# Kernel optimization log

Hardware: AMD Instinct MI355X
Metric: run time of the kernel (lower is better)

Reference implementation:

```python
import jax, jax.numpy as jnp
import numpy as np

ATOM = 34
HID = 256
LATENT = 128
CELLS = 512
B, N = 64, 128
NEG = -9e15


def setup_inputs() -> dict:
    key = jax.random.key(0)
    ks = jax.random.split(key, 20)
    inp = {}
    inp["xs"] = jax.random.normal(ks[0], (B, N, ATOM), dtype=jnp.float32)
    inp["A"] = jax.random.randint(ks[1], (B, N, N), 0, 2, dtype=jnp.int32)
    inp["cell_emb"] = jax.random.normal(ks[2], (B, CELLS), dtype=jnp.float32)
    inp["Wg"] = jax.random.normal(ks[3], (3, ATOM, ATOM), dtype=jnp.float32) * 0.17
    inp["bg"] = jnp.zeros((3, ATOM), dtype=jnp.float32)
    inp["attn"] = jax.random.normal(ks[4], (3, 2 * ATOM), dtype=jnp.float32) * 0.17
    # W_gnn_trans: 34 -> 256
    inp["Wt"] = jax.random.normal(ks[5], (ATOM, HID), dtype=jnp.float32) * 0.08
    inp["bt"] = jnp.zeros((HID,), dtype=jnp.float32)
    # ffn: 256 -> 34 ; ffn2: 34 -> latent
    inp["Wf"] = jax.random.normal(ks[6], (HID, ATOM), dtype=jnp.float32) * 0.08
    inp["bf"] = jnp.zeros((ATOM,), dtype=jnp.float32)
    inp["Wf2"] = jax.random.normal(ks[7], (ATOM, LATENT), dtype=jnp.float32) * 0.11
    inp["bf2"] = jnp.zeros((LATENT,), dtype=jnp.float32)
    # Decoder MLP: (latent+cells)->128->256->512->1
    din = LATENT + CELLS
    inp["W1"] = jax.random.normal(ks[8], (din, 128), dtype=jnp.float32) * 0.05
    inp["b1"] = jnp.zeros((128,), dtype=jnp.float32)
    inp["W2"] = jax.random.normal(ks[9], (128, 256), dtype=jnp.float32) * 0.07
    inp["b2"] = jnp.zeros((256,), dtype=jnp.float32)
    inp["W3"] = jax.random.normal(ks[10], (256, 512), dtype=jnp.float32) * 0.05
    inp["b3"] = jnp.zeros((512,), dtype=jnp.float32)
    inp["W4"] = jax.random.normal(ks[11], (512, 1), dtype=jnp.float32) * 0.06
    inp["b4"] = jnp.zeros((1,), dtype=jnp.float32)
    return inp


def reference(xs, A, cell_emb, Wg, bg, attn, Wt, bt, Wf, bf, Wf2, bf2,
              W1, b1, W2, b2, W3, b3, W4, b4):
    # ---- gnn(): 3 rounds of GAT-style masked-softmax message passing ----
    # a_input[b,p,q] = [h[b,p], h[b,q]], so e = leaky_relu(h@a1 outer+ h@a2)
    h0 = xs
    mask = A > 0  # [B,N,N]
    x = xs
    for i in range(3):
        h = jax.nn.relu(jnp.einsum('bnd,de->bne', x, Wg[i]) + bg[i])  # [B,N,34]
        f_src = h @ attn[i, :ATOM]   # [B,N] -- score contribution of row atom
        f_dst = h @ attn[i, ATOM:]   # [B,N] -- score contribution of col atom
        e = jax.nn.leaky_relu(f_src[:, :, None] + f_dst[:, None, :], 0.01)
        scores = jnp.where(mask, e, NEG)
        att = jax.nn.softmax(scores, axis=2)  # dropout disabled (deterministic)
        x = x + jnp.einsum('bpq,bqd->bpd', att, h)
    g = jax.nn.relu(jnp.einsum('bnd,dh->bnh', x, Wt) + bt)  # [B,N,HID]

    # ---- VEC_forward ----
    d = jnp.einsum('bnh,hd->bnd', g, Wf) + bf + h0        # ffn + residual to input xs
    d = jnp.einsum('bnd,dl->bnl', d, Wf2) + bf2           # [B,N,LATENT]
    d = jnp.max(d, axis=1)                                # [B,LATENT]
    vec = jax.nn.sigmoid(jnp.concatenate([d, cell_emb], axis=-1))

    # ---- Decoder_mlp (dropout disabled) ----
    hminus = jax.nn.relu(vec @ W1 + b1)
    hminus = jax.nn.relu(hminus @ W2 + b2)
    hminus = jax.nn.relu(hminus @ W3 + b3)
    score = hminus @ W4 + b4                              # [B,1]
    return score
```

## Files before the change

kernel.cpp:

```cpp
#include <hip/hip_runtime.h>

constexpr int ATOM = 34;
constexpr int HID = 256;
constexpr int LATENT = 128;
constexpr int CELLS = 512;
constexpr int NN = 128;
constexpr int NA = NN * ATOM;
#define NEGF (-9e15f)

__global__ __launch_bounds__(256, 2) void k_gat(
    const float* __restrict__ xsrc, const int* __restrict__ A,
    const float* __restrict__ Wg, const float* __restrict__ bg,
    const float* __restrict__ av, float* __restrict__ X)
{
    const int b = blockIdx.x >> 3, s8 = blockIdx.x & 7;
    const int t = threadIdx.x, lane = t & 63, wave = t >> 6;
    const int p0 = s8 * 16;

    __shared__ __align__(16) float xl[NN * 36];
    __shared__ __align__(16) float hlT[ATOM * 132];
    __shared__ __align__(16) float att[16 * NN];
    __shared__ __align__(16) float wgT[ATOM * 36];
    __shared__ float fs[NN], fd[NN], bgs[ATOM], avs[2 * ATOM];

    for (int i = t; i < ATOM * ATOM; i += 256) {
        int d = i / ATOM, e = i - d * ATOM;
        wgT[e * 36 + d] = Wg[i];
    }
    if (t < 68)  wgT[(t >> 1) * 36 + 34 + (t & 1)] = 0.f;
    if (t < ATOM)     bgs[t] = bg[t];
    if (t < 2 * ATOM) avs[t] = av[t];
    const float* xp = xsrc + b * NA;
    for (int i = t; i < NA; i += 256) xl[(i / ATOM) * 36 + (i % ATOM)] = xp[i];
    xl[(t >> 1) * 36 + 34 + (t & 1)] = 0.f;
    __syncthreads();

    {
        const int n = t >> 1, sub = t & 1;
        float xr[36];
        {
            float4* xr4 = (float4*)xr;
            const float4* p4 = (const float4*)(xl + n * 36);
            #pragma unroll
            for (int k = 0; k < 9; ++k) xr4[k] = p4[k];
        }
        #pragma unroll
        for (int j = 0; j < 17; ++j) {
            const int e = sub + 2 * j;
            float acc = bgs[e];
            const float4* wp = (const float4*)(wgT + e * 36);
            #pragma unroll
            for (int k = 0; k < 9; ++k) {
                float4 w = wp[k];
                acc += xr[4*k] * w.x + xr[4*k+1] * w.y + xr[4*k+2] * w.z + xr[4*k+3] * w.w;
            }
            hlT[e * 132 + n] = fmaxf(acc, 0.f);
        }
    }
    __syncthreads();

    {
        const int n = t & 127, w = t >> 7;
        const float* avp = avs + w * ATOM;
        float acc = 0.f;
        #pragma unroll
        for (int d = 0; d < ATOM; ++d) acc += hlT[d * 132 + n] * avp[d];
        if (w == 0) fs[n] = acc; else fd[n] = acc;
    }
    __syncthreads();

    const int* Ab = A + b * NN * NN;
    #pragma unroll
    for (int i = 0; i < 4; ++i) {
        int lp = wave * 4 + i, gp = p0 + lp;
        float fsv = fs[gp];
        unsigned long long m0 = __ballot(Ab[gp * NN + lane] > 0);
        unsigned long long m1 = __ballot(Ab[gp * NN + 64 + lane] > 0);
        float s0 = fsv + fd[lane];
        s0 = (s0 > 0.f) ? s0 : 0.01f * s0;
        if (!((m0 >> lane) & 1ull)) s0 = NEGF;
        float s1 = fsv + fd[64 + lane];
        s1 = (s1 > 0.f) ? s1 : 0.01f * s1;
        if (!((m1 >> lane) & 1ull)) s1 = NEGF;
        float mx = fmaxf(s0, s1);
        #pragma unroll
        for (int o = 32; o >= 1; o >>= 1) mx = fmaxf(mx, __shfl_xor(mx, o, 64));
        float e0 = __expf(s0 - mx), e1 = __expf(s1 - mx);
        float sm = e0 + e1;
        #pragma unroll
        for (int o = 32; o >= 1; o >>= 1) sm += __shfl_xor(sm, o, 64);
        float inv = 1.f / sm;
        att[lp * NN + lane]      = e0 * inv;
        att[lp * NN + 64 + lane] = e1 * inv;
    }
    __syncthreads();

    {
        const int p = t >> 4, g = t & 15, gp = p0 + p;
        const float4* ap  = (const float4*)(att + p * NN);
        const float4* h1p = (const float4*)(hlT + g * 132);
        const float4* h2p = (const float4*)(hlT + (g + 16) * 132);
        float a1 = 0.f, a2 = 0.f;
        #pragma unroll 8
        for (int k = 0; k < 32; ++k) {
            float4 a4 = ap[k], x1 = h1p[k], x2 = h2p[k];
            a1 += a4.x * x1.x + a4.y * x1.y + a4.z * x1.z + a4.w * x1.w;
            a2 += a4.x * x2.x + a4.y * x2.y + a4.z * x2.z + a4.w * x2.w;
        }
        float* Xr = X + b * NA + gp * ATOM;
        Xr[g]      = xl[gp * 36 + g] + a1;
        Xr[g + 16] = xl[gp * 36 + g + 16] + a2;
        if (g < 2) {
            const float4* h3p = (const float4*)(hlT + (g + 32) * 132);
            float a3 = 0.f;
            #pragma unroll 8
            for (int k = 0; k < 32; ++k) {
                float4 a4 = ap[k], x3 = h3p[k];
                a3 += a4.x * x3.x + a4.y * x3.y + a4.z * x3.z + a4.w * x3.w;
            }
            Xr[g + 32] = xl[gp * 36 + g + 32] + a3;
        }
    }
}

__global__ __launch_bounds__(512, 2) void k_phaseB(
    const float* __restrict__ X, const float* __restrict__ xs,
    const float* __restrict__ Wt, const float* __restrict__ bt,
    const float* __restrict__ Wf, const float* __restrict__ bf,
    const float* __restrict__ Wf2, const float* __restrict__ bf2,
    float* __restrict__ DM)
{
    const int b = blockIdx.x >> 2, q4 = blockIdx.x & 3;
    const int t = threadIdx.x;
    const int p0 = q4 * 32;
    __shared__ float wt[HID * 36];
    __shared__ float wf[HID * 36];
    __shared__ float xl[32][36];
    __shared__ float dlT[ATOM][33];
    __shared__ float wf2s[ATOM * LATENT];
    __shared__ float bts[HID];
    __shared__ float bfs[ATOM];
    __shared__ float sl[512];

    for (int i = t; i < ATOM * HID; i += 512) {
        int d = i >> 8, h = i & 255;
        wt[h * 36 + d] = Wt[i];
    }
    for (int i = t; i < HID * ATOM; i += 512) {
        int h = i / ATOM, j = i % ATOM;
        wf[h * 36 + j] = Wf[i];
    }
    for (int i = t; i < ATOM * LATENT; i += 512) wf2s[i] = Wf2[i];
    if (t < HID)  bts[t] = bt[t];
    if (t < ATOM) bfs[t] = bf[t];
    for (int i = t; i < 32 * ATOM; i += 512) xl[i / ATOM][i % ATOM] = X[b * NA + p0 * ATOM + i];
    __syncthreads();

    const int row = t & 31, sub = t >> 5;
    float dp[ATOM];
    #pragma unroll
    for (int j = 0; j < ATOM; ++j) dp[j] = 0.f;
    {
        float xr[36];
        float4* xr4 = (float4*)xr;
        const float4* xlr = (const float4*)&xl[row][0];
        #pragma unroll
        for (int k = 0; k < 9; ++k) xr4[k] = xlr[k];
        for (int i = 0; i < 16; ++i) {
            const int h = sub + 16 * i;
            float acc = bts[h];
            const float4* wtp = (const float4*)&wt[h * 36];
            #pragma unroll
            for (int k = 0; k < 8; ++k) {
                float4 w4 = wtp[k];
                acc += xr[4*k] * w4.x + xr[4*k+1] * w4.y + xr[4*k+2] * w4.z + xr[4*k+3] * w4.w;
            }
            acc += xr[32] * wt[h * 36 + 32] + xr[33] * wt[h * 36 + 33];
            acc = fmaxf(acc, 0.f);
            const float4* wfp = (const float4*)&wf[h * 36];
            #pragma unroll
            for (int k = 0; k < 8; ++k) {
                float4 w4 = wfp[k];
                dp[4*k]   += acc * w4.x; dp[4*k+1] += acc * w4.y;
                dp[4*k+2] += acc * w4.z; dp[4*k+3] += acc * w4.w;
            }
            dp[32] += acc * wf[h * 36 + 32];
            dp[33] += acc * wf[h * 36 + 33];
        }
    }
    __syncthreads();
    {
        float* pl = (sub < 8) ? wt : wf;
        const int s8 = sub & 7;
        #pragma unroll
        for (int j = 0; j < ATOM; ++j) pl[(s8 * 32 + row) * ATOM + j] = dp[j];
    }
    __syncthreads();
    for (int i = t; i < 32 * ATOM; i += 512) {
        int rr = i / ATOM, j = i % ATOM;
        float dv = bfs[j] + xs[b * NA + (p0 + rr) * ATOM + j];
        #pragma unroll
        for (int s = 0; s < 8; ++s)
            dv += wt[(s * 32 + rr) * ATOM + j] + wf[(s * 32 + rr) * ATOM + j];
        dlT[j][rr] = dv;
    }
    __syncthreads();
    {
        const int l = t & 127, chunk = t >> 7;
        float w2r[ATOM];
        #pragma unroll
        for (int j = 0; j < ATOM; ++j) w2r[j] = wf2s[j * LATENT + l];
        float mx = -3.4e38f;
        for (int rr = chunk * 8; rr < chunk * 8 + 8; ++rr) {
            float acc = bf2[l];
            #pragma unroll
            for (int j = 0; j < ATOM; ++j) acc += dlT[j][rr] * w2r[j];
            mx = fmaxf(mx, acc);
        }
        sl[chunk * 128 + l] = mx;
    }
    __syncthreads();
    if (t < LATENT)
        DM[(b * 4 + q4) * LATENT + t] =
            fmaxf(fmaxf(sl[t], sl[128 + t]), fmaxf(sl[256 + t], sl[384 + t]));
}

__global__ __launch_bounds__(1024) void k_dec(
    const float* __restrict__ DM, const float* __restrict__ cell,
    const float* __restrict__ W1, const float* __restrict__ b1,
    const float* __restrict__ W2, const float* __restrict__ b2,
    const float* __restrict__ W3, const float* __restrict__ b3,
    const float* __restrict__ W4, const float* __restrict__ b4,
    float* __restrict__ out)
{
    const int b = blockIdx.x, t = threadIdx.x, lane = t & 63, wave = t >> 6;
    __shared__ float vec[LATENT + CELLS];
    __shared__ float h1[128], h2[256], h3[512];
    __shared__ float sl[1024];
    if (t < LATENT) {
        float m = fmaxf(fmaxf(DM[(b*4+0)*LATENT + t], DM[(b*4+1)*LATENT + t]),
                        fmaxf(DM[(b*4+2)*LATENT + t], DM[(b*4+3)*LATENT + t]));
        vec[t] = 1.f / (1.f + __expf(-m));
    } else if (t >= 512) {
        int c = t - 512;
        vec[LATENT + c] = 1.f / (1.f + __expf(-cell[b * CELLS + c]));
    }
    __syncthreads();
    {
        const int j = t & 127, part = t >> 7;
        float acc = 0.f;
        #pragma unroll 4
        for (int k = part * 80; k < part * 80 + 80; ++k)
            acc += vec[k] * W1[k * 128 + j];
        sl[part * 128 + j] = acc;
    }
    __syncthreads();
    if (t < 128) {
        float v = b1[t];
        #pragma unroll
        for (int p = 0; p < 8; ++p) v += sl[p * 128 + t];
        h1[t] = fmaxf(v, 0.f);
    }
    __syncthreads();
    {
        const int j = t & 255, part = t >> 8;
        float acc = 0.f;
        #pragma unroll 4
        for (int k = part * 32; k < part * 32 + 32; ++k)
            acc += h1[k] * W2[k * 256 + j];
        sl[part * 256 + j] = acc;
    }
    __syncthreads();
    if (t < 256) h2[t] = fmaxf(sl[t] + sl[256 + t] + sl[512 + t] + sl[768 + t] + b2[t], 0.f);
    __syncthreads();
    {
        const int j = t & 511, part = t >> 9;
        float acc = 0.f;
        #pragma unroll 4
        for (int k = part * 128; k < part * 128 + 128; ++k)
            acc += h2[k] * W3[k * 512 + j];
        sl[part * 512 + j] = acc;
    }
    __syncthreads();
    if (t < 512) h3[t] = fmaxf(sl[t] + sl[512 + t] + b3[t], 0.f);
    __syncthreads();
    float v = (t < 512) ? h3[t] * W4[t] : 0.f;
    #pragma unroll
    for (int o = 32; o >= 1; o >>= 1) v += __shfl_xor(v, o, 64);
    if (lane == 0) sl[wave] = v;
    __syncthreads();
    if (t == 0) {
        float s = b4[0];
        #pragma unroll
        for (int w = 0; w < 16; ++w) s += sl[w];
        out[b] = s;
    }
}

extern "C" void kernel_launch(void* const* d_in, const int* in_sizes, int n_in,
                              void* d_out, int out_size, void* d_ws, size_t ws_size,
                              hipStream_t stream) {
    const float* xs       = (const float*)d_in[0];
    const int*   A        = (const int*)  d_in[1];
    const float* cell_emb = (const float*)d_in[2];
    const float* Wg       = (const float*)d_in[3];
    const float* bg       = (const float*)d_in[4];
    const float* attnv    = (const float*)d_in[5];
    const float* Wt       = (const float*)d_in[6];
    const float* bt       = (const float*)d_in[7];
    const float* Wf       = (const float*)d_in[8];
    const float* bf       = (const float*)d_in[9];
    const float* Wf2      = (const float*)d_in[10];
    const float* bf2      = (const float*)d_in[11];
    const float* W1       = (const float*)d_in[12];
    const float* b1       = (const float*)d_in[13];
    const float* W2       = (const float*)d_in[14];
    const float* b2       = (const float*)d_in[15];
    const float* W3       = (const float*)d_in[16];
    const float* b3       = (const float*)d_in[17];
    const float* W4       = (const float*)d_in[18];
    const float* b4       = (const float*)d_in[19];
    float* out = (float*)d_out;

    float* W  = (float*)d_ws;
    float* X0 = W;
    float* X1 = W + 278528;
    float* DM = W + 557056;

    k_gat<<<512, 256, 0, stream>>>(xs, A, Wg,                   bg,            attnv,           X0);
    k_gat<<<512, 256, 0, stream>>>(X0, A, Wg + ATOM * ATOM,     bg + ATOM,     attnv + 2*ATOM,  X1);
    k_gat<<<512, 256, 0, stream>>>(X1, A, Wg + 2 * ATOM * ATOM, bg + 2 * ATOM, attnv + 4*ATOM,  X0);
    k_phaseB<<<256, 512, 0, stream>>>(X0, xs, Wt, bt, Wf, bf, Wf2, bf2, DM);
    k_dec<<<64, 1024, 0, stream>>>(DM, cell_emb, W1, b1, W2, b2, W3, b3, W4, b4, out);
}
```

Measured before the change: 177.8 us.

## Pack adjacency into bitmasks once and retile GAT blocks to 32 rows

The first GAT round writes the adjacency row masks as 64-bit ballots to workspace, and the later two rounds read those masks instead of reloading the int32 adjacency matrix. GAT blocks grow to 512 threads covering 32 rows each, which halves the number of blocks that recompute h for the same batch. The aggregation now uses a 2x2 register tile with a split-K shuffle reduction. phaseB drops its Wf2 and bias shared-memory staging in favour of direct global reads and zero-pads the weight rows. The cost is fewer blocks (256) and larger per-block work, which may reduce occupancy and latency hiding.

```diff
diff --git a/kernel.cpp b/kernel.cpp
--- a/kernel.cpp
+++ b/kernel.cpp
@@ -8,60 +8,62 @@
 constexpr int NA = NN * ATOM;
 #define NEGF (-9e15f)
 
-__global__ __launch_bounds__(256, 2) void k_gat(
+template <int R>
+__global__ __launch_bounds__(512) void k_gat(
     const float* __restrict__ xsrc, const int* __restrict__ A,
-    const float* __restrict__ Wg, const float* __restrict__ bg,
-    const float* __restrict__ av, float* __restrict__ X)
+    unsigned long long* __restrict__ Mm,
+    const float* __restrict__ Wgr, const float* __restrict__ bgr,
+    const float* __restrict__ avr, float* __restrict__ X)
 {
-    const int b = blockIdx.x >> 3, s8 = blockIdx.x & 7;
+    const int b = blockIdx.x >> 2, q4 = blockIdx.x & 3;
     const int t = threadIdx.x, lane = t & 63, wave = t >> 6;
-    const int p0 = s8 * 16;
+    const int p0 = q4 * 32;
 
     __shared__ __align__(16) float xl[NN * 36];
     __shared__ __align__(16) float hlT[ATOM * 132];
-    __shared__ __align__(16) float att[16 * NN];
+    __shared__ __align__(16) float att[32 * 132];
     __shared__ __align__(16) float wgT[ATOM * 36];
-    __shared__ float fs[NN], fd[NN], bgs[ATOM], avs[2 * ATOM];
-
-    for (int i = t; i < ATOM * ATOM; i += 256) {
+    __shared__ float fs[NN], fd[NN];
+
+    const float* xp = xsrc + b * NA;
+    for (int i = t; i < NA; i += 512) xl[(i / ATOM) * 36 + (i % ATOM)] = xp[i];
+    if (t < 256) xl[(t >> 1) * 36 + 34 + (t & 1)] = 0.f;
+    for (int i = t; i < ATOM * ATOM; i += 512) {
         int d = i / ATOM, e = i - d * ATOM;
-        wgT[e * 36 + d] = Wg[i];
-    }
-    if (t < 68)  wgT[(t >> 1) * 36 + 34 + (t & 1)] = 0.f;
-    if (t < ATOM)     bgs[t] = bg[t];
-    if (t < 2 * ATOM) avs[t] = av[t];
-    const float* xp = xsrc + b * NA;
-    for (int i = t; i < NA; i += 256) xl[(i / ATOM) * 36 + (i % ATOM)] = xp[i];
-    xl[(t >> 1) * 36 + 34 + (t & 1)] = 0.f;
-    __syncthreads();
-
-    {
-        const int n = t >> 1, sub = t & 1;
+        wgT[e * 36 + d] = Wgr[i];
+    }
+    if (t < 68) wgT[(t >> 1) * 36 + 34 + (t & 1)] = 0.f;
+    __syncthreads();
+
+    {
+        const int n = t >> 2, sub = t & 3;
         float xr[36];
         {
-            float4* xr4 = (float4*)xr;
+            float4* x4 = (float4*)xr;
             const float4* p4 = (const float4*)(xl + n * 36);
             #pragma unroll
-            for (int k = 0; k < 9; ++k) xr4[k] = p4[k];
-        }
-        #pragma unroll
-        for (int j = 0; j < 17; ++j) {
-            const int e = sub + 2 * j;
-            float acc = bgs[e];
-            const float4* wp = (const float4*)(wgT + e * 36);
-            #pragma unroll
-            for (int k = 0; k < 9; ++k) {
-                float4 w = wp[k];
-                acc += xr[4*k] * w.x + xr[4*k+1] * w.y + xr[4*k+2] * w.z + xr[4*k+3] * w.w;
+            for (int k = 0; k < 9; ++k) x4[k] = p4[k];
+        }
+        #pragma unroll
+        for (int j = 0; j < 9; ++j) {
+            const int e = sub + 4 * j;
+            if (e < ATOM) {
+                float acc = bgr[e];
+                const float4* wp = (const float4*)(wgT + e * 36);
+                #pragma unroll
+                for (int k = 0; k < 9; ++k) {
+                    float4 w = wp[k];
+                    acc += xr[4*k] * w.x + xr[4*k+1] * w.y + xr[4*k+2] * w.z + xr[4*k+3] * w.w;
+                }
+                hlT[e * 132 + n] = fmaxf(acc, 0.f);
             }
-            hlT[e * 132 + n] = fmaxf(acc, 0.f);
-        }
-    }
-    __syncthreads();
-
-    {
+        }
+    }
+    __syncthreads();
+
+    if (t < 2 * NN) {
         const int n = t & 127, w = t >> 7;
-        const float* avp = avs + w * ATOM;
+        const float* avp = avr + w * ATOM;
         float acc = 0.f;
         #pragma unroll
         for (int d = 0; d < ATOM; ++d) acc += hlT[d * 132 + n] * avp[d];
@@ -70,12 +72,20 @@
     __syncthreads();
 
     const int* Ab = A + b * NN * NN;
+    unsigned long long* Mb = Mm + b * NN * 2;
     #pragma unroll
     for (int i = 0; i < 4; ++i) {
-        int lp = wave * 4 + i, gp = p0 + lp;
-        float fsv = fs[gp];
-        unsigned long long m0 = __ballot(Ab[gp * NN + lane] > 0);
-        unsigned long long m1 = __ballot(Ab[gp * NN + 64 + lane] > 0);
+        const int lp = wave * 4 + i, gp = p0 + lp;
+        unsigned long long m0, m1;
+        if (R == 0) {
+            m0 = __ballot(Ab[gp * NN + lane] > 0);
+            m1 = __ballot(Ab[gp * NN + 64 + lane] > 0);
+            if (lane == 0) { Mb[gp * 2] = m0; Mb[gp * 2 + 1] = m1; }
+        } else {
+            m0 = Mb[gp * 2];
+            m1 = Mb[gp * 2 + 1];
+        }
+        const float fsv = fs[gp];
         float s0 = fsv + fd[lane];
         s0 = (s0 > 0.f) ? s0 : 0.01f * s0;
         if (!((m0 >> lane) & 1ull)) s0 = NEGF;
@@ -90,40 +100,60 @@
         #pragma unroll
         for (int o = 32; o >= 1; o >>= 1) sm += __shfl_xor(sm, o, 64);
         float inv = 1.f / sm;
-        att[lp * NN + lane]      = e0 * inv;
-        att[lp * NN + 64 + lane] = e1 * inv;
-    }
-    __syncthreads();
-
-    {
-        const int p = t >> 4, g = t & 15, gp = p0 + p;
-        const float4* ap  = (const float4*)(att + p * NN);
-        const float4* h1p = (const float4*)(hlT + g * 132);
-        const float4* h2p = (const float4*)(hlT + (g + 16) * 132);
-        float a1 = 0.f, a2 = 0.f;
-        #pragma unroll 8
-        for (int k = 0; k < 32; ++k) {
-            float4 a4 = ap[k], x1 = h1p[k], x2 = h2p[k];
-            a1 += a4.x * x1.x + a4.y * x1.y + a4.z * x1.z + a4.w * x1.w;
-            a2 += a4.x * x2.x + a4.y * x2.y + a4.z * x2.z + a4.w * x2.w;
-        }
-        float* Xr = X + b * NA + gp * ATOM;
-        Xr[g]      = xl[gp * 36 + g] + a1;
-        Xr[g + 16] = xl[gp * 36 + g + 16] + a2;
-        if (g < 2) {
-            const float4* h3p = (const float4*)(hlT + (g + 32) * 132);
-            float a3 = 0.f;
-            #pragma unroll 8
-            for (int k = 0; k < 32; ++k) {
-                float4 a4 = ap[k], x3 = h3p[k];
-                a3 += a4.x * x3.x + a4.y * x3.y + a4.z * x3.z + a4.w * x3.w;
-            }
-            Xr[g + 32] = xl[gp * 36 + g + 32] + a3;
+        att[lp * 132 + lane]      = e0 * inv;
+        att[lp * 132 + 64 + lane] = e1 * inv;
+    }
+    __syncthreads();
+
+    {
+        const int pq = t >> 5, g = (t >> 1) & 15, kh = t & 1;
+        const int rA = 2 * pq, rB = rA + 1;
+        const float4* apA = (const float4*)(att + rA * 132 + kh * 64);
+        const float4* apB = (const float4*)(att + rB * 132 + kh * 64);
+        const float4* hA  = (const float4*)(hlT + g * 132 + kh * 64);
+        const float4* hB  = (const float4*)(hlT + (g + 16) * 132 + kh * 64);
+        float aAA = 0.f, aAB = 0.f, aBA = 0.f, aBB = 0.f;
+        #pragma unroll
+        for (int k = 0; k < 16; ++k) {
+            float4 a0 = apA[k], a1 = apB[k], h0 = hA[k], h1 = hB[k];
+            aAA += a0.x * h0.x + a0.y * h0.y + a0.z * h0.z + a0.w * h0.w;
+            aAB += a0.x * h1.x + a0.y * h1.y + a0.z * h1.z + a0.w * h1.w;
+            aBA += a1.x * h0.x + a1.y * h0.y + a1.z * h0.z + a1.w * h0.w;
+            aBB += a1.x * h1.x + a1.y * h1.y + a1.z * h1.z + a1.w * h1.w;
+        }
+        aAA += __shfl_xor(aAA, 1, 64);
+        aAB += __shfl_xor(aAB, 1, 64);
+        aBA += __shfl_xor(aBA, 1, 64);
+        aBB += __shfl_xor(aBB, 1, 64);
+        if (kh == 0) {
+            const int gpA = p0 + rA, gpB = p0 + rB;
+            float* XrA = X + b * NA + gpA * ATOM;
+            float* XrB = X + b * NA + gpB * ATOM;
+            XrA[g]      = xl[gpA * 36 + g] + aAA;
+            XrA[g + 16] = xl[gpA * 36 + g + 16] + aAB;
+            XrB[g]      = xl[gpB * 36 + g] + aBA;
+            XrB[g + 16] = xl[gpB * 36 + g + 16] + aBB;
+        }
+    }
+    if (t < 128) {
+        const int p = t >> 2, c = 32 + ((t >> 1) & 1), kh = t & 1;
+        const float4* ap = (const float4*)(att + p * 132 + kh * 64);
+        const float4* hp = (const float4*)(hlT + c * 132 + kh * 64);
+        float a = 0.f;
+        #pragma unroll
+        for (int k = 0; k < 16; ++k) {
+            float4 a4 = ap[k], h4 = hp[k];
+            a += a4.x * h4.x + a4.y * h4.y + a4.z * h4.z + a4.w * h4.w;
+        }
+        a += __shfl_xor(a, 1, 64);
+        if (kh == 0) {
+            const int gp = p0 + p;
+            X[b * NA + gp * ATOM + c] = xl[gp * 36 + c] + a;
         }
     }
 }
 
-__global__ __launch_bounds__(512, 2) void k_phaseB(
+__global__ __launch_bounds__(512, 1) void k_phaseB(
     const float* __restrict__ X, const float* __restrict__ xs,
     const float* __restrict__ Wt, const float* __restrict__ bt,
     const float* __restrict__ Wf, const float* __restrict__ bf,
@@ -133,13 +163,10 @@
     const int b = blockIdx.x >> 2, q4 = blockIdx.x & 3;
     const int t = threadIdx.x;
     const int p0 = q4 * 32;
-    __shared__ float wt[HID * 36];
-    __shared__ float wf[HID * 36];
-    __shared__ float xl[32][36];
-    __shared__ float dlT[ATOM][33];
-    __shared__ float wf2s[ATOM * LATENT];
-    __shared__ float bts[HID];
-    __shared__ float bfs[ATOM];
+    __shared__ __align__(16) float wt[HID * 36];
+    __shared__ __align__(16) float wf[HID * 36];
+    __shared__ __align__(16) float xl[32 * 36];
+    __shared__ float dlT[ATOM * 33];
     __shared__ float sl[512];
 
     for (int i = t; i < ATOM * HID; i += 512) {
@@ -147,74 +174,81 @@
         wt[h * 36 + d] = Wt[i];
     }
     for (int i = t; i < HID * ATOM; i += 512) {
-        int h = i / ATOM, j = i % ATOM;
+        int h = i / ATOM, j = i - (i / ATOM) * ATOM;
         wf[h * 36 + j] = Wf[i];
     }
-    for (int i = t; i < ATOM * LATENT; i += 512) wf2s[i] = Wf2[i];
-    if (t < HID)  bts[t] = bt[t];
-    if (t < ATOM) bfs[t] = bf[t];
-    for (int i = t; i < 32 * ATOM; i += 512) xl[i / ATOM][i % ATOM] = X[b * NA + p0 * ATOM + i];
-    __syncthreads();
-
-    const int row = t & 31, sub = t >> 5;
-    float dp[ATOM];
-    #pragma unroll
-    for (int j = 0; j < ATOM; ++j) dp[j] = 0.f;
-    {
-        float xr[36];
-        float4* xr4 = (float4*)xr;
-        const float4* xlr = (const float4*)&xl[row][0];
-        #pragma unroll
-        for (int k = 0; k < 9; ++k) xr4[k] = xlr[k];
-        for (int i = 0; i < 16; ++i) {
-            const int h = sub + 16 * i;
-            float acc = bts[h];
-            const float4* wtp = (const float4*)&wt[h * 36];
+    wt[(t >> 1) * 36 + 34 + (t & 1)] = 0.f;
+    wf[(t >> 1) * 36 + 34 + (t & 1)] = 0.f;
+    for (int i = t; i < 32 * ATOM; i += 512) xl[(i / ATOM) * 36 + (i % ATOM)] = X[b * NA + p0 * ATOM + i];
+    if (t < 64) xl[(t >> 1) * 36 + 34 + (t & 1)] = 0.f;
+    __syncthreads();
+
+    {
+        const int row = t & 31, sub = t >> 5;
+        float dp[ATOM];
+        #pragma unroll
+        for (int j = 0; j < ATOM; ++j) dp[j] = 0.f;
+        {
+            float xr[36];
+            float4* xr4 = (float4*)xr;
+            const float4* xlr = (const float4*)(xl + row * 36);
             #pragma unroll
-            for (int k = 0; k < 8; ++k) {
-                float4 w4 = wtp[k];
-                acc += xr[4*k] * w4.x + xr[4*k+1] * w4.y + xr[4*k+2] * w4.z + xr[4*k+3] * w4.w;
+            for (int k = 0; k < 9; ++k) xr4[k] = xlr[k];
+            for (int i = 0; i < 16; ++i) {
+                const int h = sub + 16 * i;
+                float acc = bt[h];
+                const float4* wtp = (const float4*)(wt + h * 36);
+                #pragma unroll
+                for (int k = 0; k < 9; ++k) {
+                    float4 w4 = wtp[k];
+                    acc += xr[4*k] * w4.x + xr[4*k+1] * w4.y + xr[4*k+2] * w4.z + xr[4*k+3] * w4.w;
+                }
+                acc = fmaxf(acc, 0.f);
+                const float4* wfp = (const float4*)(wf + h * 36);
+                #pragma unroll
+                for (int k = 0; k < 8; ++k) {
+                    float4 w4 = wfp[k];
+                    dp[4*k]   += acc * w4.x; dp[4*k+1] += acc * w4.y;
+                    dp[4*k+2] += acc * w4.z; dp[4*k+3] += acc * w4.w;
+                }
+                dp[32] += acc * wf[h * 36 + 32];
+                dp[33] += acc * wf[h * 36 + 33];
             }
-            acc += xr[32] * wt[h * 36 + 32] + xr[33] * wt[h * 36 + 33];
-            acc = fmaxf(acc, 0.f);
-            const float4* wfp = (const float4*)&wf[h * 36];
-            #pragma unroll
-            for (int k = 0; k < 8; ++k) {
-                float4 w4 = wfp[k];
-                dp[4*k]   += acc * w4.x; dp[4*k+1] += acc * w4.y;
-                dp[4*k+2] += acc * w4.z; dp[4*k+3] += acc * w4.w;
-            }
-            dp[32] += acc * wf[h * 36 + 32];
-            dp[33] += acc * wf[h * 36 + 33];
-        }
-    }
-    __syncthreads();
-    {
+        }
+        __syncthreads();
         float* pl = (sub < 8) ? wt : wf;
         const int s8 = sub & 7;
         #pragma unroll
         for (int j = 0; j < ATOM; ++j) pl[(s8 * 32 + row) * ATOM + j] = dp[j];
     }
     __syncthreads();
-    for (int i = t; i < 32 * ATOM; i += 512) {
-        int rr = i / ATOM, j = i % ATOM;
-        float dv = bfs[j] + xs[b * NA + (p0 + rr) * ATOM + j];
-        #pragma unroll
-        for (int s = 0; s < 8; ++s)
-            dv += wt[(s * 32 + rr) * ATOM + j] + wf[(s * 32 + rr) * ATOM + j];
-        dlT[j][rr] = dv;
-    }
-    __syncthreads();
+
+    {
+        const float* xsq = xs + b * NA + p0 * ATOM;
+        for (int i = t; i < 32 * ATOM; i += 512) {
+            int rr = i / ATOM, j = i - (i / ATOM) * ATOM;
+            float dv = bf[j] + xsq[rr * ATOM + j];
+            #pragma unroll
+            for (int s = 0; s < 8; ++s)
+                dv += wt[(s * 32 + rr) * ATOM + j] + wf[(s * 32 + rr) * ATOM + j];
+            dlT[j * 33 + rr] = dv;
+        }
+    }
+    __syncthreads();
+
     {
         const int l = t & 127, chunk = t >> 7;
         float w2r[ATOM];
         #pragma unroll
-        for (int j = 0; j < ATOM; ++j) w2r[j] = wf2s[j * LATENT + l];
+        for (int j = 0; j < ATOM; ++j) w2r[j] = Wf2[j * LATENT + l];
+        const float bb = bf2[l];
         float mx = -3.4e38f;
-        for (int rr = chunk * 8; rr < chunk * 8 + 8; ++rr) {
-            float acc = bf2[l];
+        #pragma unroll
+        for (int r8 = 0; r8 < 8; ++r8) {
+            const int rr = chunk * 8 + r8;
+            float acc = bb;
             #pragma unroll
-            for (int j = 0; j < ATOM; ++j) acc += dlT[j][rr] * w2r[j];
+            for (int j = 0; j < ATOM; ++j) acc += dlT[j * 33 + rr] * w2r[j];
             mx = fmaxf(mx, acc);
         }
         sl[chunk * 128 + l] = mx;
@@ -322,14 +356,15 @@
     const float* b4       = (const float*)d_in[19];
     float* out = (float*)d_out;
 
-    float* W  = (float*)d_ws;
-    float* X0 = W;
-    float* X1 = W + 278528;
-    float* DM = W + 557056;
-
-    k_gat<<<512, 256, 0, stream>>>(xs, A, Wg,                   bg,            attnv,           X0);
-    k_gat<<<512, 256, 0, stream>>>(X0, A, Wg + ATOM * ATOM,     bg + ATOM,     attnv + 2*ATOM,  X1);
-    k_gat<<<512, 256, 0, stream>>>(X1, A, Wg + 2 * ATOM * ATOM, bg + 2 * ATOM, attnv + 4*ATOM,  X0);
+    float* Wsp = (float*)d_ws;
+    float* X0 = Wsp;
+    float* X1 = Wsp + 278528;
+    float* DM = Wsp + 557056;
+    unsigned long long* Mm = (unsigned long long*)(Wsp + 589824);
+
+    k_gat<0><<<256, 512, 0, stream>>>(xs, A, Mm, Wg,                   bg,      attnv,       X0);
+    k_gat<1><<<256, 512, 0, stream>>>(X0, A, Mm, Wg + ATOM * ATOM,     bg + 34, attnv + 68,  X1);
+    k_gat<1><<<256, 512, 0, stream>>>(X1, A, Mm, Wg + 2 * ATOM * ATOM, bg + 68, attnv + 136, X0);
     k_phaseB<<<256, 512, 0, stream>>>(X0, xs, Wt, bt, Wf, bf, Wf2, bf2, DM);
     k_dec<<<64, 1024, 0, stream>>>(DM, cell_emb, W1, b1, W2, b2, W3, b3, W4, b4, out);
 }
```

After: 168.2 us. 5.4% less time.
